# Kernel tuning notes

Hardware: AMD Instinct MI355X
Metric: run time of the kernel (lower is better)

## Reference

```python
import jax, jax.numpy as jnp
import numpy as np

B, T, C = 2, 2048, 2048
H, G, HS = 16, 4, 128       # n_head, n_query_groups, head_size
N_ELEM = 128                # rotary_percentage * head_size
D_FF = 4 * C
EPS = 1e-5


def layer_norm(x, w, b):
    mu = jnp.mean(x, axis=-1, keepdims=True)
    var = jnp.var(x, axis=-1, keepdims=True)
    return (x - mu) * jax.lax.rsqrt(var + EPS) * w + b


def apply_rope(x, cos, sin):
    # x: (B, H, T, n_elem); cos/sin: (T, n_elem) with freqs duplicated over halves
    half = x.shape[-1] // 2
    x1, x2 = x[..., :half], x[..., half:]
    rotated = jnp.concatenate((-x2, x1), axis=-1)
    return x * cos + rotated * sin


def setup_inputs() -> dict:
    key = jax.random.key(0)
    ks = jax.random.split(key, 8)
    x = jax.random.normal(ks[0], (B, T, C), dtype=jnp.float32)
    # RoPE cache (neox/llama style, duplicated halves to match half-rotation apply_rope)
    inv_freq = 1.0 / (10000.0 ** (jnp.arange(0, N_ELEM, 2, dtype=jnp.float32) / N_ELEM))
    freqs = jnp.outer(jnp.arange(T, dtype=jnp.float32), inv_freq)  # (T, n_elem/2)
    cos = jnp.concatenate((jnp.cos(freqs), jnp.cos(freqs)), axis=-1)
    sin = jnp.concatenate((jnp.sin(freqs), jnp.sin(freqs)), axis=-1)
    mask = jnp.tril(jnp.ones((T, T), dtype=bool))
    s = 0.02
    qkv_w = jax.random.normal(ks[1], ((H + 2 * G) * HS, C), dtype=jnp.float32) * s
    proj_w = jax.random.normal(ks[2], (C, C), dtype=jnp.float32) * s
    fc1_w = jax.random.normal(ks[3], (D_FF, C), dtype=jnp.float32) * s
    fc2_w = jax.random.normal(ks[4], (C, D_FF), dtype=jnp.float32) * s
    return {
        "x": x, "cos": cos, "sin": sin, "mask": mask,
        "ln1_w": jnp.ones((C,), jnp.float32), "ln1_b": jnp.zeros((C,), jnp.float32),
        "qkv_w": qkv_w, "proj_w": proj_w,
        "ln2_w": jnp.ones((C,), jnp.float32), "ln2_b": jnp.zeros((C,), jnp.float32),
        "fc1_w": fc1_w, "fc1_b": jnp.zeros((D_FF,), jnp.float32),
        "fc2_w": fc2_w, "fc2_b": jnp.zeros((C,), jnp.float32),
    }


def block_forward(x, cos, sin, mask, ln1_w, ln1_b, qkv_w, proj_w,
                  ln2_w, ln2_b, fc1_w, fc1_b, fc2_w, fc2_b):
    q_per_kv = H // G
    # --- LayerNormLinear: LN then fused QKV projection ---
    qkv = layer_norm(x, ln1_w, ln1_b) @ qkv_w.T            # (B, T, (H+2G)*HS)
    qkv = qkv.reshape(B, T, G, q_per_kv + 2, HS).transpose(0, 2, 3, 1, 4)
    q = qkv[:, :, :q_per_kv]                               # (B, G, q_per_kv, T, HS)
    k = qkv[:, :, q_per_kv:q_per_kv + 1]                   # (B, G, 1, T, HS)
    v = qkv[:, :, q_per_kv + 1:]
    # GQA expansion (repeat_interleave over the per-group axis)
    k = jnp.repeat(k, q_per_kv, axis=2)
    v = jnp.repeat(v, q_per_kv, axis=2)
    q = q.reshape(B, H, T, HS)
    k = k.reshape(B, H, T, HS)
    v = v.reshape(B, H, T, HS)
    # --- RoPE on first N_ELEM channels ---
    q = jnp.concatenate((apply_rope(q[..., :N_ELEM], cos, sin), q[..., N_ELEM:]), axis=-1)
    k = jnp.concatenate((apply_rope(k[..., :N_ELEM], cos, sin), k[..., N_ELEM:]), axis=-1)
    # --- SDPA with boolean mask ---
    scale = 1.0 / jnp.sqrt(jnp.asarray(HS, q.dtype))
    att = jnp.einsum("bhqd,bhkd->bhqk", q, k) * scale
    att = jnp.where(mask, att, jnp.finfo(att.dtype).min)
    att = jax.nn.softmax(att, axis=-1)
    y = jnp.einsum("bhqk,bhkd->bhqd", att, v)
    y = y.transpose(0, 2, 1, 3).reshape(B, T, C)
    h = y @ proj_w.T
    # --- non-parallel residual: x += attn; x += MLP(LN(x)) ---
    x = x + h
    mlp = jax.nn.gelu(layer_norm(x, ln2_w, ln2_b) @ fc1_w.T + fc1_b, approximate=False)
    x = x + (mlp @ fc2_w.T + fc2_b)
    return x


def reference(x, cos, sin, mask, ln1_w, ln1_b, qkv_w, proj_w,
              ln2_w, ln2_b, fc1_w, fc1_b, fc2_w, fc2_b):
    return block_forward(x, cos, sin, mask, ln1_w, ln1_b, qkv_w, proj_w,
                         ln2_w, ln2_b, fc1_w, fc1_b, fc2_w, fc2_b)
```

## Files before the change

### kernel.cpp

```cpp
#include <hip/hip_runtime.h>

typedef __bf16 bf16;
typedef __bf16 bf16x8 __attribute__((ext_vector_type(8)));
typedef __bf16 bf16x4 __attribute__((ext_vector_type(4)));
typedef float  f32x4  __attribute__((ext_vector_type(4)));

#define LOG2E 1.4426950408889634f

__device__ __forceinline__ void gload_lds16(const void* g, void* l) {
    __builtin_amdgcn_global_load_lds(
        (__attribute__((address_space(1))) const void*)g,
        (__attribute__((address_space(3))) void*)l, 16, 0, 0);
}

__global__ __launch_bounds__(256) void cvt_bf16(const float* __restrict__ src,
                                                bf16* __restrict__ dst, int n) {
    int i = (blockIdx.x * 256 + threadIdx.x) * 4;
    if (i + 3 < n) {
        float4 v = *(const float4*)(src + i);
        bf16x4 o;
        o[0] = (bf16)v.x; o[1] = (bf16)v.y; o[2] = (bf16)v.z; o[3] = (bf16)v.w;
        *(bf16x4*)(dst + i) = o;
    }
}

__global__ __launch_bounds__(256) void ln_kernel(const float* __restrict__ x,
                                                 const float* __restrict__ wgt,
                                                 const float* __restrict__ bias,
                                                 bf16* __restrict__ out) {
    __shared__ float red[8];
    const int tid = threadIdx.x;
    const int lane = tid & 63, w = tid >> 6;
    const size_t row = blockIdx.x;
    const float4* xr = (const float4*)(x + row * 2048);
    float4 v0 = xr[tid];
    float4 v1 = xr[tid + 256];
    float s = v0.x + v0.y + v0.z + v0.w + v1.x + v1.y + v1.z + v1.w;
    float q = v0.x*v0.x + v0.y*v0.y + v0.z*v0.z + v0.w*v0.w
            + v1.x*v1.x + v1.y*v1.y + v1.z*v1.z + v1.w*v1.w;
    #pragma unroll
    for (int off = 32; off; off >>= 1) {
        s += __shfl_xor(s, off);
        q += __shfl_xor(q, off);
    }
    if (lane == 0) { red[w] = s; red[4 + w] = q; }
    __syncthreads();
    float S  = red[0] + red[1] + red[2] + red[3];
    float Q2 = red[4] + red[5] + red[6] + red[7];
    float mu = S * (1.0f / 2048.0f);
    float var = Q2 * (1.0f / 2048.0f) - mu * mu;
    float rstd = rsqrtf(var + 1e-5f);

    bf16* orow = out + row * 2048;
    int c0 = tid * 4;
    float vv[8] = {v0.x, v0.y, v0.z, v0.w, v1.x, v1.y, v1.z, v1.w};
    bf16x4 o;
    #pragma unroll
    for (int k = 0; k < 4; ++k)
        o[k] = (bf16)((vv[k] - mu) * rstd * wgt[c0 + k] + bias[c0 + k]);
    *(bf16x4*)(orow + c0) = o;
    #pragma unroll
    for (int k = 0; k < 4; ++k)
        o[k] = (bf16)((vv[4 + k] - mu) * rstd * wgt[1024 + c0 + k] + bias[1024 + c0 + k]);
    *(bf16x4*)(orow + 1024 + c0) = o;
}

template <int EPI>
__global__ __launch_bounds__(512, 4) void gemmB(const bf16* __restrict__ A,
                                                const bf16* __restrict__ B,
                                                void* __restrict__ OutP,
                                                const float* __restrict__ bias,
                                                const float* __restrict__ res,
                                                int M, int N, int K) {
    __shared__ __align__(16) char lds[65536];
    const int tid = threadIdx.x;
    const int lane = tid & 63;
    const int w = tid >> 6, wr = w >> 1, wc = w & 1;
    const int lo = lane & 15, hi = lane >> 4;

    const int nwg = gridDim.x;
    const int bid = blockIdx.x;
    const int q = nwg >> 3, r = nwg & 7, xcd = bid & 7, off = bid >> 3;
    const int s = (xcd < r ? xcd * (q + 1) : r * (q + 1) + (xcd - r) * q) + off;
    const int MB = M / 128;
    const int per = MB * 4;
    const int grp = s / per, t2 = s - grp * per;
    const int brow = (t2 % MB) * 128;
    const int bcol = (grp * 4 + t2 / MB) * 128;

    const int sr = tid >> 3;
    const int su = (tid & 7) ^ (sr & 7);
    const bf16* Ag = A + (size_t)(brow + sr) * K + su * 8;
    const bf16* Bg = B + (size_t)(bcol + sr) * K + su * 8;
    const size_t K64 = (size_t)64 * K;
    char* dst0 = lds + tid * 16;

    auto stage = [&](int bf, int kt) {
        char* d = dst0 + bf * 32768;
        gload_lds16(Ag + kt * 64, d);
        gload_lds16(Ag + K64 + kt * 64, d + 8192);
        gload_lds16(Bg + kt * 64, d + 16384);
        gload_lds16(Bg + K64 + kt * 64, d + 24576);
    };

    f32x4 acc[2][4] = {};
    const int NT = K >> 6;

    stage(0, 0);
    for (int kt = 0; kt < NT; ++kt) {
        const int cur = kt & 1;
        if (kt + 1 < NT) {
            stage(cur ^ 1, kt + 1);
            asm volatile("s_waitcnt vmcnt(4)" ::: "memory");
        } else {
            asm volatile("s_waitcnt vmcnt(0)" ::: "memory");
        }
        __builtin_amdgcn_s_barrier();

        const char* ab = lds + cur * 32768;
        const char* bb = ab + 16384;
        bf16x8 af[2][2], bfv[4][2];
        #pragma unroll
        for (int m = 0; m < 2; ++m) {
            const int rA = wr * 32 + m * 16 + lo;
            #pragma unroll
            for (int ks = 0; ks < 2; ++ks)
                af[m][ks] = *(const bf16x8*)(ab + rA * 128 + (((ks * 4 + hi) ^ (lo & 7)) << 4));
        }
        #pragma unroll
        for (int n = 0; n < 4; ++n) {
            const int rB = wc * 64 + n * 16 + lo;
            #pragma unroll
            for (int ks = 0; ks < 2; ++ks)
                bfv[n][ks] = *(const bf16x8*)(bb + rB * 128 + (((ks * 4 + hi) ^ (lo & 7)) << 4));
        }
        __builtin_amdgcn_s_setprio(1);
        #pragma unroll
        for (int m = 0; m < 2; ++m)
            #pragma unroll
            for (int n = 0; n < 4; ++n)
                #pragma unroll
                for (int ks = 0; ks < 2; ++ks)
                    acc[m][n] = __builtin_amdgcn_mfma_f32_16x16x32_bf16(af[m][ks], bfv[n][ks], acc[m][n], 0, 0, 0);
        __builtin_amdgcn_s_setprio(0);
        __builtin_amdgcn_s_barrier();
    }

    float* outF = (float*)OutP;
    bf16*  outB = (bf16*)OutP;
    #pragma unroll
    for (int n = 0; n < 4; ++n) {
        const int col = bcol + wc * 64 + n * 16 + lo;
        float bv = 0.f;
        if (EPI == 1 || EPI == 3) bv = bias[col];
        #pragma unroll
        for (int m = 0; m < 2; ++m) {
            #pragma unroll
            for (int rr = 0; rr < 4; ++rr) {
                const int row = brow + wr * 32 + m * 16 + hi * 4 + rr;
                float v = acc[m][n][rr];
                if (EPI == 0) {
                    outB[(size_t)row * N + col] = (bf16)v;
                } else if (EPI == 1) {
                    v += bv;
                    v = 0.5f * v * (1.0f + erff(v * 0.70710678118654752f));
                    outB[(size_t)row * N + col] = (bf16)v;
                } else if (EPI == 2) {
                    outF[(size_t)row * N + col] = res[(size_t)row * N + col] + v;
                } else {
                    outF[(size_t)row * N + col] = res[(size_t)row * N + col] + v + bv;
                }
            }
        }
    }
}

__global__ __launch_bounds__(256) void rope_scatter(const bf16* __restrict__ qkv,
                                                    const float* __restrict__ cosb,
                                                    const float* __restrict__ sinb,
                                                    bf16* __restrict__ Q,
                                                    bf16* __restrict__ Kg,
                                                    bf16* __restrict__ Vt) {
    const int tid = threadIdx.x;
    const int row = blockIdx.x;
    const int b = row >> 11, t = row & 2047;
    const bf16* src = qkv + (size_t)row * 3072;
    for (int i = tid; i < 1536; i += 256) {
        int slot = i >> 6;
        int d = i & 63;
        int g = slot / 6, m = slot - g * 6;
        float v1 = (float)src[slot * 128 + d];
        float v2 = (float)src[slot * 128 + d + 64];
        float o1, o2;
        if (m < 5) {
            float c1 = cosb[t * 128 + d],      s1 = sinb[t * 128 + d];
            float c2 = cosb[t * 128 + d + 64], s2 = sinb[t * 128 + d + 64];
            o1 = v1 * c1 - v2 * s1;
            o2 = v2 * c2 + v1 * s2;
        } else {
            o1 = v1; o2 = v2;
        }
        if (m < 4) {
            int hh = g * 4 + m;
            size_t base = ((size_t)(b * 16 + hh) * 2048 + t) * 128;
            Q[base + d] = (bf16)o1;
            Q[base + d + 64] = (bf16)o2;
        } else if (m == 4) {
            size_t base = ((size_t)(b * 4 + g) * 2048 + t) * 128;
            Kg[base + d] = (bf16)o1;
            Kg[base + d + 64] = (bf16)o2;
        } else {
            size_t base = (size_t)(b * 4 + g) * 128;
            Vt[(base + d) * 2048 + t] = (bf16)o1;
            Vt[(base + d + 64) * 2048 + t] = (bf16)o2;
        }
    }
}

__global__ __launch_bounds__(256) void attn_kernel(const bf16* __restrict__ Q,
                                                   const bf16* __restrict__ Kg,
                                                   const bf16* __restrict__ Vt,
                                                   bf16* __restrict__ Y) {
    __shared__ __align__(16) bf16 Ks[64 * 128];
    __shared__ __align__(16) bf16 Vs[128 * 64];
    __shared__ __align__(16) bf16 Ps[4][16 * 80];

    const int tid = threadIdx.x;
    const int lane = tid & 63, w = tid >> 6;
    const int lo = lane & 15, hi = lane >> 4;
    const int bh = blockIdx.y;
    const int b = bh >> 4, h = bh & 15;
    const int g = h >> 2;

    const bf16* Kbase = Kg + (size_t)(b * 4 + g) * 2048 * 128;
    const bf16* Vbase = Vt + (size_t)(b * 4 + g) * 128 * 2048;
    const float scale = 0.08838834764831845f;
    bf16* pw = &Ps[w][0];

    #pragma unroll 1
    for (int pass = 0; pass < 2; ++pass) {
        const int qt = pass ? 31 - (int)blockIdx.x : (int)blockIdx.x;
        const int q0 = qt * 64;

        bf16x8 qf[4];
        {
            const size_t qbase = ((size_t)bh * 2048 + q0 + w * 16 + lo) * 128;
            #pragma unroll
            for (int dd = 0; dd < 4; ++dd)
                qf[dd] = *(const bf16x8*)(Q + qbase + dd * 32 + hi * 8);
        }

        float m_r[4], l_r[4];
        f32x4 oacc[8] = {};
        #pragma unroll
        for (int rr = 0; rr < 4; ++rr) { m_r[rr] = -1e30f; l_r[rr] = 0.f; }

        for (int kt = 0; kt <= qt; ++kt) {
            #pragma unroll
            for (int it = 0; it < 4; ++it) {
                int ob = (it * 256 + tid) * 16;
                int rk = ob >> 8, cb = ob & 255;
                bf16x8 kv = *(const bf16x8*)(Kbase + (size_t)(kt * 64 + rk) * 128 + (cb >> 1));
                *(bf16x8*)((char*)Ks + rk * 256 + (cb ^ ((rk & 7) << 4))) = kv;
                int dv = ob >> 7, cv = ob & 127;
                bf16x8 vv = *(const bf16x8*)(Vbase + (size_t)dv * 2048 + kt * 64 + (cv >> 1));
                *(bf16x8*)((char*)Vs + dv * 128 + (cv ^ ((dv & 7) << 4))) = vv;
            }
            __syncthreads();

            f32x4 sj[4];
            #pragma unroll
            for (int j = 0; j < 4; ++j) {
                f32x4 a = {};
                int rk = j * 16 + lo;
                #pragma unroll
                for (int dd = 0; dd < 4; ++dd) {
                    int cb = dd * 64 + hi * 16;
                    bf16x8 kf = *(const bf16x8*)((const char*)Ks + rk * 256 + (cb ^ ((rk & 7) << 4)));
                    a = __builtin_amdgcn_mfma_f32_16x16x32_bf16(qf[dd], kf, a, 0, 0, 0);
                }
                sj[j] = a;
            }

            float sv[4][4];
            const bool diag = (kt == qt);
            #pragma unroll
            for (int j = 0; j < 4; ++j)
                #pragma unroll
                for (int rr = 0; rr < 4; ++rr) {
                    float v = sj[j][rr] * scale;
                    if (diag) {
                        int tg = kt * 64 + j * 16 + lo;
                        int qg = q0 + w * 16 + hi * 4 + rr;
                        if (tg > qg) v = -1e30f;
                    }
                    sv[j][rr] = v;
                }

            float mx[4];
            #pragma unroll
            for (int rr = 0; rr < 4; ++rr) {
                float m0 = fmaxf(fmaxf(sv[0][rr], sv[1][rr]), fmaxf(sv[2][rr], sv[3][rr]));
                #pragma unroll
                for (int off = 8; off; off >>= 1) m0 = fmaxf(m0, __shfl_xor(m0, off, 16));
                mx[rr] = m0;
            }
            float p[4][4];
            float rs[4], al[4];
            #pragma unroll
            for (int rr = 0; rr < 4; ++rr) {
                float mnew = fmaxf(m_r[rr], mx[rr]);
                #pragma unroll
                for (int j = 0; j < 4; ++j)
                    p[j][rr] = exp2f((sv[j][rr] - mnew) * LOG2E);
                float s0 = p[0][rr] + p[1][rr] + p[2][rr] + p[3][rr];
                #pragma unroll
                for (int off = 8; off; off >>= 1) s0 += __shfl_xor(s0, off, 16);
                rs[rr] = s0;
                al[rr] = exp2f((m_r[rr] - mnew) * LOG2E);
                l_r[rr] = l_r[rr] * al[rr] + rs[rr];
                m_r[rr] = mnew;
            }
            #pragma unroll
            for (int dn = 0; dn < 8; ++dn)
                #pragma unroll
                for (int rr = 0; rr < 4; ++rr) oacc[dn][rr] *= al[rr];

            #pragma unroll
            for (int j = 0; j < 4; ++j)
                #pragma unroll
                for (int rr = 0; rr < 4; ++rr)
                    pw[(hi * 4 + rr) * 80 + j * 16 + lo] = (bf16)p[j][rr];

            #pragma unroll
            for (int tc = 0; tc < 2; ++tc) {
                bf16x8 pf = *(const bf16x8*)(pw + lo * 80 + tc * 32 + hi * 8);
                #pragma unroll
                for (int dn = 0; dn < 8; ++dn) {
                    int rv = dn * 16 + lo;
                    int cv = tc * 64 + hi * 16;
                    bf16x8 vf = *(const bf16x8*)((const char*)Vs + rv * 128 + (cv ^ ((rv & 7) << 4)));
                    oacc[dn] = __builtin_amdgcn_mfma_f32_16x16x32_bf16(pf, vf, oacc[dn], 0, 0, 0);
                }
            }
            __syncthreads();
        }

        #pragma unroll
        for (int dn = 0; dn < 8; ++dn)
            #pragma unroll
            for (int rr = 0; rr < 4; ++rr) {
                int qg = q0 + w * 16 + hi * 4 + rr;
                Y[((size_t)b * 2048 + qg) * 2048 + h * 128 + dn * 16 + lo] =
                    (bf16)(oacc[dn][rr] / l_r[rr]);
            }
    }
}

extern "C" void kernel_launch(void* const* d_in, const int* in_sizes, int n_in,
                              void* d_out, int out_size, void* d_ws, size_t ws_size,
                              hipStream_t stream) {
    const float* x      = (const float*)d_in[0];
    const float* cosb   = (const float*)d_in[1];
    const float* sinb   = (const float*)d_in[2];
    const float* ln1_w  = (const float*)d_in[4];
    const float* ln1_b  = (const float*)d_in[5];
    const float* qkv_w  = (const float*)d_in[6];
    const float* proj_w = (const float*)d_in[7];
    const float* ln2_w  = (const float*)d_in[8];
    const float* ln2_b  = (const float*)d_in[9];
    const float* fc1_w  = (const float*)d_in[10];
    const float* fc1_b  = (const float*)d_in[11];
    const float* fc2_w  = (const float*)d_in[12];
    const float* fc2_b  = (const float*)d_in[13];
    float* out = (float*)d_out;

    char* ws = (char*)d_ws;
    bf16*  w_qkv  = (bf16*)(ws + 0ull);
    bf16*  w_proj = (bf16*)(ws + 12582912ull);
    bf16*  w_fc1  = (bf16*)(ws + 20971520ull);
    bf16*  w_fc2  = (bf16*)(ws + 54525952ull);
    float* x2     = (float*)(ws + 88080384ull);
    bf16*  lnout  = (bf16*)(ws + 121634816ull);
    char*  R      = ws + 138412032ull;
    bf16*  qkvo = (bf16*)(R);
    bf16*  Qb   = (bf16*)(R + 25165824ull);
    bf16*  Kb   = (bf16*)(R + 41943040ull);
    bf16*  Vtb  = (bf16*)(R + 46137344ull);
    bf16*  Yb   = (bf16*)(R + 50331648ull);
    bf16*  mlp  = (bf16*)(R);

    cvt_bf16<<<6144,  256, 0, stream>>>(qkv_w,  w_qkv,  3072 * 2048);
    cvt_bf16<<<4096,  256, 0, stream>>>(proj_w, w_proj, 2048 * 2048);
    cvt_bf16<<<16384, 256, 0, stream>>>(fc1_w,  w_fc1,  8192 * 2048);
    cvt_bf16<<<16384, 256, 0, stream>>>(fc2_w,  w_fc2,  2048 * 8192);

    ln_kernel<<<4096, 256, 0, stream>>>(x, ln1_w, ln1_b, lnout);

    gemmB<0><<<768, 512, 0, stream>>>(lnout, w_qkv, qkvo, nullptr, nullptr,
                                      4096, 3072, 2048);

    rope_scatter<<<4096, 256, 0, stream>>>(qkvo, cosb, sinb, Qb, Kb, Vtb);

    attn_kernel<<<dim3(16, 32), 256, 0, stream>>>(Qb, Kb, Vtb, Yb);

    gemmB<2><<<512, 512, 0, stream>>>(Yb, w_proj, x2, nullptr, x,
                                      4096, 2048, 2048);

    ln_kernel<<<4096, 256, 0, stream>>>(x2, ln2_w, ln2_b, lnout);

    gemmB<1><<<2048, 512, 0, stream>>>(lnout, w_fc1, mlp, fc1_b, nullptr,
                                       4096, 8192, 2048);

    gemmB<3><<<512, 512, 0, stream>>>(mlp, w_fc2, out, fc2_b, x2,
                                      4096, 2048, 8192);
}
```

Baseline: 716.7 us.

## Add 256x256 ping-pong GEMM with split-K for fc2 and use it for QKV/fc1/fc2

Introduces a new GEMM kernel with 256x256 tiles, 128KB dynamic LDS double buffering, explicit barrier/waitcnt interleaving of LDS reads, global-to-LDS loads and MFMA quarters, plus s_setprio around MFMA bursts. It replaces the previous GEMM for the QKV, fc1 and fc2 projections. fc2 is split into two K halves across blockIdx.y, with the second half written to a scratch buffer and summed by a separate add kernel. The goal is more data reuse per tile and better latency hiding, and the split-K keeps fc2's small grid filling the GPU. The cost is an extra fp32 pass for the split-K reduction, reduced occupancy, and reuse of the fc1 weight workspace as scratch.

```diff
diff --git a/kernel.cpp b/kernel.cpp
--- a/kernel.cpp
+++ b/kernel.cpp
@@ -12,6 +12,16 @@
         (__attribute__((address_space(1))) const void*)g,
         (__attribute__((address_space(3))) void*)l, 16, 0, 0);
 }
+
+template <int N> __device__ __forceinline__ void vmwait() {
+    if constexpr (N == 0) asm volatile("s_waitcnt vmcnt(0)" ::: "memory");
+    else if constexpr (N == 4) asm volatile("s_waitcnt vmcnt(4)" ::: "memory");
+}
+
+#define BARA() { asm volatile("" ::: "memory"); __builtin_amdgcn_s_barrier(); \
+    asm volatile("s_waitcnt lgkmcnt(0)" ::: "memory"); __builtin_amdgcn_sched_barrier(0); }
+#define BARB() { asm volatile("" ::: "memory"); __builtin_amdgcn_s_barrier(); \
+    asm volatile("" ::: "memory"); }
 
 __global__ __launch_bounds__(256) void cvt_bf16(const float* __restrict__ src,
                                                 bf16* __restrict__ dst, int n) {
@@ -21,6 +31,17 @@
         bf16x4 o;
         o[0] = (bf16)v.x; o[1] = (bf16)v.y; o[2] = (bf16)v.z; o[3] = (bf16)v.w;
         *(bf16x4*)(dst + i) = o;
+    }
+}
+
+__global__ __launch_bounds__(256) void add_f32(float* __restrict__ out,
+                                               const float* __restrict__ p, int n) {
+    int i = (blockIdx.x * 256 + threadIdx.x) * 4;
+    if (i + 3 < n) {
+        float4 a = *(const float4*)(out + i);
+        float4 b = *(const float4*)(p + i);
+        a.x += b.x; a.y += b.y; a.z += b.z; a.w += b.w;
+        *(float4*)(out + i) = a;
     }
 }
 
@@ -63,6 +84,141 @@
     for (int k = 0; k < 4; ++k)
         o[k] = (bf16)((vv[4 + k] - mu) * rstd * wgt[1024 + c0 + k] + bias[1024 + c0 + k]);
     *(bf16x4*)(orow + 1024 + c0) = o;
+}
+
+template <int EPI>
+__global__ __launch_bounds__(512, 2) void gemmP(const bf16* __restrict__ A,
+                                                const bf16* __restrict__ B,
+                                                void* __restrict__ OutP,
+                                                const float* __restrict__ bias,
+                                                const float* __restrict__ res,
+                                                float* __restrict__ Aux,
+                                                int M, int N, int Kc,
+                                                int lda, int ldb) {
+    extern __shared__ __align__(16) char lds[];
+    const int tid = threadIdx.x;
+    const int lane = tid & 63;
+    const int w = tid >> 6, wr = w >> 2, wc = w & 3;
+    const int lo = lane & 15, hi = lane >> 4;
+    const int ln16 = lane * 16;
+    const int koff = (EPI == 5) ? (int)blockIdx.y * Kc : 0;
+
+    const int nwg = gridDim.x;
+    const int bid = blockIdx.x;
+    const int q = nwg >> 3, r = nwg & 7, xcd = bid & 7, off = bid >> 3;
+    const int s = (xcd < r ? xcd * (q + 1) : r * (q + 1) + (xcd - r) * q) + off;
+    const int MB = M / 256;
+    const int per = MB * 4;
+    const int grp = s / per, t2 = s - grp * per;
+    const int brow = (t2 % MB) * 256;
+    const int bcol = (grp * 4 + t2 / MB) * 256;
+
+    const bf16* Asrc = A + (size_t)(brow + w * 16 + lo) * lda + koff + hi * 8;
+    const bf16* Bsrc = B + (size_t)(bcol + w * 16 + lo) * ldb + koff + hi * 8;
+
+    auto stA = [&](int bf, int kt, int h) {
+        const bf16* g = Asrc + (size_t)h * 128 * lda + kt * 64;
+        char* d = lds + bf * 65536 + h * 16384 + (w << 10) + ln16;
+        gload_lds16(g, d);
+        gload_lds16(g + 32, d + 8192);
+    };
+    auto stB = [&](int bf, int kt, int h) {
+        const bf16* g = Bsrc + (size_t)h * 128 * ldb + kt * 64;
+        char* d = lds + bf * 65536 + 32768 + h * 16384 + (w << 10) + ln16;
+        gload_lds16(g, d);
+        gload_lds16(g + 32, d + 8192);
+    };
+
+    bf16x8 af[4][2], b0[2][2], b1[2][2];
+    f32x4 acc[8][4] = {};
+
+#define LDA(BF, MH) { _Pragma("unroll") for (int mm = 0; mm < 4; ++mm) { \
+    _Pragma("unroll") for (int ks = 0; ks < 2; ++ks) { \
+        af[mm][ks] = *(const bf16x8*)(lds + (BF) * 65536 + wr * 16384 + \
+                                      ((ks * 8 + (MH) * 4 + mm) << 10) + ln16); } } }
+#define LDB(BF, NH, RG) { _Pragma("unroll") for (int nn = 0; nn < 2; ++nn) { \
+    _Pragma("unroll") for (int ks = 0; ks < 2; ++ks) { \
+        RG[nn][ks] = *(const bf16x8*)(lds + (BF) * 65536 + 32768 + (wc >> 1) * 16384 + \
+                                      ((ks * 8 + (wc & 1) * 4 + (NH) * 2 + nn) << 10) + ln16); } } }
+#define MFMAQ(MH, NH, RG) { __builtin_amdgcn_s_setprio(1); \
+    _Pragma("unroll") for (int mm = 0; mm < 4; ++mm) { \
+    _Pragma("unroll") for (int nn = 0; nn < 2; ++nn) { \
+    _Pragma("unroll") for (int ks = 0; ks < 2; ++ks) { \
+        acc[(MH) * 4 + mm][(NH) * 2 + nn] = __builtin_amdgcn_mfma_f32_16x16x32_bf16( \
+            af[mm][ks], RG[nn][ks], acc[(MH) * 4 + mm][(NH) * 2 + nn], 0, 0, 0); } } } \
+    __builtin_amdgcn_s_setprio(0); }
+
+    const int NT = Kc >> 6;
+    const int NIT = NT >> 1;
+
+    stA(0, 0, 0); stA(0, 0, 1);
+    stB(0, 0, 0); stB(0, 0, 1);
+    stA(1, 1, 0); stA(1, 1, 1);
+    vmwait<4>();
+    BARB();
+
+    #pragma unroll 1
+    for (int T = 0; T < NIT - 1; ++T) {
+        const int t = 2 * T;
+        LDA(0, 0) LDB(0, 0, b0) stB(1, t + 1, 0); stB(1, t + 1, 1);
+        BARA(); MFMAQ(0, 0, b0) BARB();
+        LDB(0, 1, b1)  BARA(); MFMAQ(0, 1, b1) BARB();
+        LDA(0, 1)      BARA(); MFMAQ(1, 1, b1) BARB();
+        LDB(0, 0, b0)  stA(0, t + 2, 0); stA(0, t + 2, 1); vmwait<4>();
+        BARA(); MFMAQ(1, 0, b0) BARB();
+        LDA(1, 0) LDB(1, 0, b0) stB(0, t + 2, 0); stB(0, t + 2, 1);
+        BARA(); MFMAQ(0, 0, b0) BARB();
+        LDB(1, 1, b1)  BARA(); MFMAQ(0, 1, b1) BARB();
+        LDA(1, 1)      BARA(); MFMAQ(1, 1, b1) BARB();
+        LDB(1, 0, b0)  stA(1, t + 3, 0); stA(1, t + 3, 1); vmwait<4>();
+        BARA(); MFMAQ(1, 0, b0) BARB();
+    }
+    {
+        LDA(0, 0) LDB(0, 0, b0) stB(1, NT - 1, 0); stB(1, NT - 1, 1);
+        BARA(); MFMAQ(0, 0, b0) BARB();
+        LDB(0, 1, b1)  BARA(); MFMAQ(0, 1, b1) BARB();
+        LDA(0, 1)      BARA(); MFMAQ(1, 1, b1) BARB();
+        LDB(0, 0, b0)  vmwait<0>();
+        BARA(); MFMAQ(1, 0, b0) BARB();
+        LDA(1, 0) LDB(1, 0, b0) BARA(); MFMAQ(0, 0, b0) BARB();
+        LDB(1, 1, b1)  BARA(); MFMAQ(0, 1, b1) BARB();
+        LDA(1, 1)      BARA(); MFMAQ(1, 1, b1) BARB();
+        LDB(1, 0, b0)  BARA(); MFMAQ(1, 0, b0)
+    }
+#undef LDA
+#undef LDB
+#undef MFMAQ
+
+    float* outF = (float*)OutP;
+    bf16*  outB = (bf16*)OutP;
+    #pragma unroll
+    for (int n = 0; n < 4; ++n) {
+        const int col = bcol + wc * 64 + n * 16 + lo;
+        float bv = 0.f;
+        if (EPI == 1 || EPI == 3 || EPI == 5) bv = bias[col];
+        #pragma unroll
+        for (int m = 0; m < 8; ++m) {
+            #pragma unroll
+            for (int rr = 0; rr < 4; ++rr) {
+                const int row = brow + wr * 128 + m * 16 + hi * 4 + rr;
+                float v = acc[m][n][rr];
+                if (EPI == 0) {
+                    outB[(size_t)row * N + col] = (bf16)v;
+                } else if (EPI == 1) {
+                    v += bv;
+                    v = 0.5f * v * (1.0f + erff(v * 0.70710678118654752f));
+                    outB[(size_t)row * N + col] = (bf16)v;
+                } else if (EPI == 3) {
+                    outF[(size_t)row * N + col] = res[(size_t)row * N + col] + v + bv;
+                } else if (EPI == 5) {
+                    if (blockIdx.y == 0)
+                        outF[(size_t)row * N + col] = res[(size_t)row * N + col] + v + bv;
+                    else
+                        Aux[(size_t)row * N + col] = v;
+                }
+            }
+        }
+    }
 }
 
 template <int EPI>
@@ -389,6 +545,7 @@
     bf16*  Vtb  = (bf16*)(R + 46137344ull);
     bf16*  Yb   = (bf16*)(R + 50331648ull);
     bf16*  mlp  = (bf16*)(R);
+    float* p1   = (float*)(ws + 20971520ull);
 
     cvt_bf16<<<6144,  256, 0, stream>>>(qkv_w,  w_qkv,  3072 * 2048);
     cvt_bf16<<<4096,  256, 0, stream>>>(proj_w, w_proj, 2048 * 2048);
@@ -397,8 +554,8 @@
 
     ln_kernel<<<4096, 256, 0, stream>>>(x, ln1_w, ln1_b, lnout);
 
-    gemmB<0><<<768, 512, 0, stream>>>(lnout, w_qkv, qkvo, nullptr, nullptr,
-                                      4096, 3072, 2048);
+    gemmP<0><<<dim3(192, 1), 512, 131072, stream>>>(lnout, w_qkv, qkvo, nullptr, nullptr,
+                                                    nullptr, 4096, 3072, 2048, 2048, 2048);
 
     rope_scatter<<<4096, 256, 0, stream>>>(qkvo, cosb, sinb, Qb, Kb, Vtb);
 
@@ -409,9 +566,10 @@
 
     ln_kernel<<<4096, 256, 0, stream>>>(x2, ln2_w, ln2_b, lnout);
 
-    gemmB<1><<<2048, 512, 0, stream>>>(lnout, w_fc1, mlp, fc1_b, nullptr,
-                                       4096, 8192, 2048);
-
-    gemmB<3><<<512, 512, 0, stream>>>(mlp, w_fc2, out, fc2_b, x2,
-                                      4096, 2048, 8192);
-}
+    gemmP<1><<<dim3(512, 1), 512, 131072, stream>>>(lnout, w_fc1, mlp, fc1_b, nullptr,
+                                                    nullptr, 4096, 8192, 2048, 2048, 2048);
+
+    gemmP<5><<<dim3(128, 2), 512, 131072, stream>>>(mlp, w_fc2, out, fc2_b, x2,
+                                                    p1, 4096, 2048, 4096, 8192, 8192);
+    add_f32<<<8192, 256, 0, stream>>>(out, p1, 4096 * 2048);
+}
```

New measurement: 754.9 us. +5.3%, slower.

## Use 256x256-tile GEMM for FC1 and split V transpose into dedicated kernel

Applied to the files above, without the earlier changes.

Adds a new GEMM kernel with 256x256 output tiles, 8x4 MFMA accumulators per wave, double-buffered direct-to-LDS loads, XCD-aware block remapping and setprio around MFMA bursts. It replaces the FC1+GELU GEMM, aiming for more operand reuse and fewer workgroups. Separately, the V transpose moves out of rope_scatter into a kernel that writes 16-byte vector stores instead of strided scalar scatters. The large tile raises register pressure and uses 64KB of LDS per block, which may limit occupancy.

```diff
diff --git a/kernel.cpp b/kernel.cpp
--- a/kernel.cpp
+++ b/kernel.cpp
@@ -175,45 +175,157 @@
     }
 }
 
+template <int EPI>
+__global__ __launch_bounds__(512, 2) void gemmE(const bf16* __restrict__ A,
+                                                const bf16* __restrict__ B,
+                                                void* __restrict__ OutP,
+                                                const float* __restrict__ bias,
+                                                int M, int N, int K) {
+    extern __shared__ __align__(16) char lds[];
+    const int tid = threadIdx.x;
+    const int lane = tid & 63;
+    const int w = tid >> 6, wr = w >> 2, wc = w & 3;
+    const int lo = lane & 15, hi = lane >> 4;
+
+    const int nwg = gridDim.x;
+    const int bid = blockIdx.x;
+    const int q = nwg >> 3, r = nwg & 7, xcd = bid & 7, off = bid >> 3;
+    const int s = (xcd < r ? xcd * (q + 1) : r * (q + 1) + (xcd - r) * q) + off;
+    const int MB = M / 256;
+    const int per = MB * 4;
+    const int grp = s / per, t2 = s - grp * per;
+    const int brow = (t2 % MB) * 256;
+    const int bcol = (grp * 4 + t2 / MB) * 256;
+
+    const int srow = tid >> 2;
+    const int scol = ((tid & 3) ^ ((tid >> 3) & 3)) * 8;
+    const bf16* Ag = A + (size_t)(brow + srow) * K + scol;
+    const bf16* Bg = B + (size_t)(bcol + srow) * K + scol;
+    const size_t R128 = (size_t)128 * K;
+    char* d0 = lds + tid * 16;
+
+    auto stage = [&](int bf, int kt) {
+        char* d = d0 + bf * 32768;
+        gload_lds16(Ag + kt * 32, d);
+        gload_lds16(Ag + R128 + kt * 32, d + 8192);
+        gload_lds16(Bg + kt * 32, d + 16384);
+        gload_lds16(Bg + R128 + kt * 32, d + 24576);
+    };
+
+    f32x4 acc[8][4] = {};
+    const int NT = K >> 5;
+    const int xsl = (hi ^ ((lo >> 1) & 3)) << 4;
+
+    stage(0, 0);
+    #pragma unroll 1
+    for (int kt = 0; kt < NT; ++kt) {
+        const int cur = kt & 1;
+        if (kt + 1 < NT) {
+            stage(cur ^ 1, kt + 1);
+            asm volatile("s_waitcnt vmcnt(4)" ::: "memory");
+        } else {
+            asm volatile("s_waitcnt vmcnt(0)" ::: "memory");
+        }
+        __builtin_amdgcn_s_barrier();
+
+        const char* ab = lds + cur * 32768;
+        const char* bb = ab + 16384;
+        bf16x8 af[8], bv[4];
+        #pragma unroll
+        for (int m = 0; m < 4; ++m)
+            af[m] = *(const bf16x8*)(ab + (wr * 128 + m * 16 + lo) * 64 + xsl);
+        #pragma unroll
+        for (int n = 0; n < 4; ++n)
+            bv[n] = *(const bf16x8*)(bb + (wc * 64 + n * 16 + lo) * 64 + xsl);
+        __builtin_amdgcn_s_setprio(1);
+        #pragma unroll
+        for (int m = 0; m < 4; ++m)
+            #pragma unroll
+            for (int n = 0; n < 4; ++n)
+                acc[m][n] = __builtin_amdgcn_mfma_f32_16x16x32_bf16(af[m], bv[n], acc[m][n], 0, 0, 0);
+        __builtin_amdgcn_s_setprio(0);
+        #pragma unroll
+        for (int m = 4; m < 8; ++m)
+            af[m] = *(const bf16x8*)(ab + (wr * 128 + m * 16 + lo) * 64 + xsl);
+        __builtin_amdgcn_s_setprio(1);
+        #pragma unroll
+        for (int m = 4; m < 8; ++m)
+            #pragma unroll
+            for (int n = 0; n < 4; ++n)
+                acc[m][n] = __builtin_amdgcn_mfma_f32_16x16x32_bf16(af[m], bv[n], acc[m][n], 0, 0, 0);
+        __builtin_amdgcn_s_setprio(0);
+        __builtin_amdgcn_s_barrier();
+    }
+
+    bf16* outB = (bf16*)OutP;
+    #pragma unroll
+    for (int n = 0; n < 4; ++n) {
+        const int col = bcol + wc * 64 + n * 16 + lo;
+        float bv2 = bias[col];
+        #pragma unroll
+        for (int m = 0; m < 8; ++m) {
+            #pragma unroll
+            for (int rr = 0; rr < 4; ++rr) {
+                const int row = brow + wr * 128 + m * 16 + hi * 4 + rr;
+                float v = acc[m][n][rr] + bv2;
+                v = 0.5f * v * (1.0f + erff(v * 0.70710678118654752f));
+                outB[(size_t)row * N + col] = (bf16)v;
+            }
+        }
+    }
+}
+
 __global__ __launch_bounds__(256) void rope_scatter(const bf16* __restrict__ qkv,
                                                     const float* __restrict__ cosb,
                                                     const float* __restrict__ sinb,
                                                     bf16* __restrict__ Q,
-                                                    bf16* __restrict__ Kg,
-                                                    bf16* __restrict__ Vt) {
+                                                    bf16* __restrict__ Kg) {
     const int tid = threadIdx.x;
     const int row = blockIdx.x;
     const int b = row >> 11, t = row & 2047;
     const bf16* src = qkv + (size_t)row * 3072;
-    for (int i = tid; i < 1536; i += 256) {
+    #pragma unroll
+    for (int i = tid; i < 1280; i += 256) {
         int slot = i >> 6;
         int d = i & 63;
-        int g = slot / 6, m = slot - g * 6;
-        float v1 = (float)src[slot * 128 + d];
-        float v2 = (float)src[slot * 128 + d + 64];
-        float o1, o2;
-        if (m < 5) {
-            float c1 = cosb[t * 128 + d],      s1 = sinb[t * 128 + d];
-            float c2 = cosb[t * 128 + d + 64], s2 = sinb[t * 128 + d + 64];
-            o1 = v1 * c1 - v2 * s1;
-            o2 = v2 * c2 + v1 * s2;
-        } else {
-            o1 = v1; o2 = v2;
-        }
+        int g = slot / 5, m = slot - g * 5;
+        int msrc = g * 6 + m;
+        float v1 = (float)src[msrc * 128 + d];
+        float v2 = (float)src[msrc * 128 + d + 64];
+        float c1 = cosb[t * 128 + d],      s1 = sinb[t * 128 + d];
+        float c2 = cosb[t * 128 + d + 64], s2 = sinb[t * 128 + d + 64];
+        float o1 = v1 * c1 - v2 * s1;
+        float o2 = v2 * c2 + v1 * s2;
         if (m < 4) {
             int hh = g * 4 + m;
             size_t base = ((size_t)(b * 16 + hh) * 2048 + t) * 128;
             Q[base + d] = (bf16)o1;
             Q[base + d + 64] = (bf16)o2;
-        } else if (m == 4) {
+        } else {
             size_t base = ((size_t)(b * 4 + g) * 2048 + t) * 128;
             Kg[base + d] = (bf16)o1;
             Kg[base + d + 64] = (bf16)o2;
-        } else {
-            size_t base = (size_t)(b * 4 + g) * 128;
-            Vt[(base + d) * 2048 + t] = (bf16)o1;
-            Vt[(base + d + 64) * 2048 + t] = (bf16)o2;
-        }
+        }
+    }
+}
+
+__global__ __launch_bounds__(256) void vtrans(const bf16* __restrict__ qkvo,
+                                              bf16* __restrict__ Vt) {
+    const int tid = threadIdx.x;
+    const int t0 = blockIdx.x * 64;
+    const int z  = blockIdx.y;
+    const int b = z >> 2, g = z & 3;
+    const int d = tid & 127;
+    const int th = tid >> 7;
+    const bf16* src = qkvo + (size_t)(b * 2048 + t0 + th * 32) * 3072 + g * 768 + 640 + d;
+    bf16* dst = Vt + ((size_t)z * 128 + d) * 2048 + t0 + th * 32;
+    #pragma unroll
+    for (int c = 0; c < 4; ++c) {
+        bf16x8 v;
+        #pragma unroll
+        for (int j = 0; j < 8; ++j)
+            v[j] = src[(size_t)(c * 8 + j) * 3072];
+        *(bf16x8*)(dst + c * 8) = v;
     }
 }
 
@@ -390,6 +502,8 @@
     bf16*  Yb   = (bf16*)(R + 50331648ull);
     bf16*  mlp  = (bf16*)(R);
 
+    constexpr int LDSE = 65536;
+
     cvt_bf16<<<6144,  256, 0, stream>>>(qkv_w,  w_qkv,  3072 * 2048);
     cvt_bf16<<<4096,  256, 0, stream>>>(proj_w, w_proj, 2048 * 2048);
     cvt_bf16<<<16384, 256, 0, stream>>>(fc1_w,  w_fc1,  8192 * 2048);
@@ -400,7 +514,8 @@
     gemmB<0><<<768, 512, 0, stream>>>(lnout, w_qkv, qkvo, nullptr, nullptr,
                                       4096, 3072, 2048);
 
-    rope_scatter<<<4096, 256, 0, stream>>>(qkvo, cosb, sinb, Qb, Kb, Vtb);
+    rope_scatter<<<4096, 256, 0, stream>>>(qkvo, cosb, sinb, Qb, Kb);
+    vtrans<<<dim3(32, 8), 256, 0, stream>>>(qkvo, Vtb);
 
     attn_kernel<<<dim3(16, 32), 256, 0, stream>>>(Qb, Kb, Vtb, Yb);
 
@@ -409,8 +524,8 @@
 
     ln_kernel<<<4096, 256, 0, stream>>>(x2, ln2_w, ln2_b, lnout);
 
-    gemmB<1><<<2048, 512, 0, stream>>>(lnout, w_fc1, mlp, fc1_b, nullptr,
-                                       4096, 8192, 2048);
+    gemmE<1><<<512, 512, LDSE, stream>>>(lnout, w_fc1, mlp, fc1_b,
+                                         4096, 8192, 2048);
 
     gemmB<3><<<512, 512, 0, stream>>>(mlp, w_fc2, out, fc2_b, x2,
                                       4096, 2048, 8192);
```

After: 706.6 us. Within noise of the previous version (-1.4%).

## Double-buffer attention K/V tiles, lazy softmax rescale, split V transpose kernel

Applied to the files above, without the earlier changes.

The attention kernel now double-buffers K and V in LDS. It prefetches the next tile into registers while computing the current one, which drops one barrier per iteration and hides global load latency. The online softmax now rescales the accumulator only when a row max grows by more than a threshold. This skips exp and multiply work on most tiles, at the cost of slightly different numerics that should still stay bounded. The strided V-transpose writes are moved out of rope_scatter into a separate vtrans kernel that writes contiguous 16-byte chunks, at the cost of one extra kernel launch.

```diff
diff --git a/kernel.cpp b/kernel.cpp
--- a/kernel.cpp
+++ b/kernel.cpp
@@ -179,41 +179,53 @@
                                                     const float* __restrict__ cosb,
                                                     const float* __restrict__ sinb,
                                                     bf16* __restrict__ Q,
-                                                    bf16* __restrict__ Kg,
-                                                    bf16* __restrict__ Vt) {
+                                                    bf16* __restrict__ Kg) {
     const int tid = threadIdx.x;
     const int row = blockIdx.x;
     const int b = row >> 11, t = row & 2047;
     const bf16* src = qkv + (size_t)row * 3072;
-    for (int i = tid; i < 1536; i += 256) {
+    #pragma unroll
+    for (int i = tid; i < 1280; i += 256) {
         int slot = i >> 6;
         int d = i & 63;
-        int g = slot / 6, m = slot - g * 6;
-        float v1 = (float)src[slot * 128 + d];
-        float v2 = (float)src[slot * 128 + d + 64];
-        float o1, o2;
-        if (m < 5) {
-            float c1 = cosb[t * 128 + d],      s1 = sinb[t * 128 + d];
-            float c2 = cosb[t * 128 + d + 64], s2 = sinb[t * 128 + d + 64];
-            o1 = v1 * c1 - v2 * s1;
-            o2 = v2 * c2 + v1 * s2;
-        } else {
-            o1 = v1; o2 = v2;
-        }
+        int g = slot / 5, m = slot - g * 5;
+        int msrc = g * 6 + m;
+        float v1 = (float)src[msrc * 128 + d];
+        float v2 = (float)src[msrc * 128 + d + 64];
+        float c1 = cosb[t * 128 + d],      s1 = sinb[t * 128 + d];
+        float c2 = cosb[t * 128 + d + 64], s2 = sinb[t * 128 + d + 64];
+        float o1 = v1 * c1 - v2 * s1;
+        float o2 = v2 * c2 + v1 * s2;
         if (m < 4) {
             int hh = g * 4 + m;
             size_t base = ((size_t)(b * 16 + hh) * 2048 + t) * 128;
             Q[base + d] = (bf16)o1;
             Q[base + d + 64] = (bf16)o2;
-        } else if (m == 4) {
+        } else {
             size_t base = ((size_t)(b * 4 + g) * 2048 + t) * 128;
             Kg[base + d] = (bf16)o1;
             Kg[base + d + 64] = (bf16)o2;
-        } else {
-            size_t base = (size_t)(b * 4 + g) * 128;
-            Vt[(base + d) * 2048 + t] = (bf16)o1;
-            Vt[(base + d + 64) * 2048 + t] = (bf16)o2;
-        }
+        }
+    }
+}
+
+__global__ __launch_bounds__(256) void vtrans(const bf16* __restrict__ qkvo,
+                                              bf16* __restrict__ Vt) {
+    const int tid = threadIdx.x;
+    const int t0 = blockIdx.x * 64;
+    const int z  = blockIdx.y;
+    const int b = z >> 2, g = z & 3;
+    const int d = tid & 127;
+    const int th = tid >> 7;
+    const bf16* src = qkvo + (size_t)(b * 2048 + t0 + th * 32) * 3072 + g * 768 + 640 + d;
+    bf16* dst = Vt + ((size_t)z * 128 + d) * 2048 + t0 + th * 32;
+    #pragma unroll
+    for (int c = 0; c < 4; ++c) {
+        bf16x8 v;
+        #pragma unroll
+        for (int j = 0; j < 8; ++j)
+            v[j] = src[(size_t)(c * 8 + j) * 3072];
+        *(bf16x8*)(dst + c * 8) = v;
     }
 }
 
@@ -221,8 +233,8 @@
                                                    const bf16* __restrict__ Kg,
                                                    const bf16* __restrict__ Vt,
                                                    bf16* __restrict__ Y) {
-    __shared__ __align__(16) bf16 Ks[64 * 128];
-    __shared__ __align__(16) bf16 Vs[128 * 64];
+    __shared__ __align__(16) bf16 Ks[2][64 * 128];
+    __shared__ __align__(16) bf16 Vs[2][128 * 64];
     __shared__ __align__(16) bf16 Ps[4][16 * 80];
 
     const int tid = threadIdx.x;
@@ -237,6 +249,8 @@
     const float scale = 0.08838834764831845f;
     bf16* pw = &Ps[w][0];
 
+    bf16x8 kreg[4], vreg[4];
+
     #pragma unroll 1
     for (int pass = 0; pass < 2; ++pass) {
         const int qt = pass ? 31 - (int)blockIdx.x : (int)blockIdx.x;
@@ -255,18 +269,40 @@
         #pragma unroll
         for (int rr = 0; rr < 4; ++rr) { m_r[rr] = -1e30f; l_r[rr] = 0.f; }
 
+        #pragma unroll
+        for (int it = 0; it < 4; ++it) {
+            int ob = (it * 256 + tid) * 16;
+            int rk = ob >> 8, cb = ob & 255;
+            kreg[it] = *(const bf16x8*)(Kbase + (size_t)rk * 128 + (cb >> 1));
+            int dv = ob >> 7, cv = ob & 127;
+            vreg[it] = *(const bf16x8*)(Vbase + (size_t)dv * 2048 + (cv >> 1));
+        }
+        #pragma unroll
+        for (int it = 0; it < 4; ++it) {
+            int ob = (it * 256 + tid) * 16;
+            int rk = ob >> 8, cb = ob & 255;
+            *(bf16x8*)((char*)Ks[0] + rk * 256 + (cb ^ ((rk & 7) << 4))) = kreg[it];
+            int dv = ob >> 7, cv = ob & 127;
+            *(bf16x8*)((char*)Vs[0] + dv * 128 + (cv ^ ((dv & 7) << 4))) = vreg[it];
+        }
+        __syncthreads();
+        int cur = 0;
+
         for (int kt = 0; kt <= qt; ++kt) {
-            #pragma unroll
-            for (int it = 0; it < 4; ++it) {
-                int ob = (it * 256 + tid) * 16;
-                int rk = ob >> 8, cb = ob & 255;
-                bf16x8 kv = *(const bf16x8*)(Kbase + (size_t)(kt * 64 + rk) * 128 + (cb >> 1));
-                *(bf16x8*)((char*)Ks + rk * 256 + (cb ^ ((rk & 7) << 4))) = kv;
-                int dv = ob >> 7, cv = ob & 127;
-                bf16x8 vv = *(const bf16x8*)(Vbase + (size_t)dv * 2048 + kt * 64 + (cv >> 1));
-                *(bf16x8*)((char*)Vs + dv * 128 + (cv ^ ((dv & 7) << 4))) = vv;
-            }
-            __syncthreads();
+            const bool pf = (kt < qt);
+            if (pf) {
+                #pragma unroll
+                for (int it = 0; it < 4; ++it) {
+                    int ob = (it * 256 + tid) * 16;
+                    int rk = ob >> 8, cb = ob & 255;
+                    kreg[it] = *(const bf16x8*)(Kbase + (size_t)((kt + 1) * 64 + rk) * 128 + (cb >> 1));
+                    int dv = ob >> 7, cv = ob & 127;
+                    vreg[it] = *(const bf16x8*)(Vbase + (size_t)dv * 2048 + (kt + 1) * 64 + (cv >> 1));
+                }
+            }
+
+            const char* KsC = (const char*)Ks[cur];
+            const char* VsC = (const char*)Vs[cur];
 
             f32x4 sj[4];
             #pragma unroll
@@ -276,7 +312,7 @@
                 #pragma unroll
                 for (int dd = 0; dd < 4; ++dd) {
                     int cb = dd * 64 + hi * 16;
-                    bf16x8 kf = *(const bf16x8*)((const char*)Ks + rk * 256 + (cb ^ ((rk & 7) << 4)));
+                    bf16x8 kf = *(const bf16x8*)(KsC + rk * 256 + (cb ^ ((rk & 7) << 4)));
                     a = __builtin_amdgcn_mfma_f32_16x16x32_bf16(qf[dd], kf, a, 0, 0, 0);
                 }
                 sj[j] = a;
@@ -305,26 +341,33 @@
                 for (int off = 8; off; off >>= 1) m0 = fmaxf(m0, __shfl_xor(m0, off, 16));
                 mx[rr] = m0;
             }
+
+            bool need = false;
+            #pragma unroll
+            for (int rr = 0; rr < 4; ++rr) need = need || (mx[rr] > m_r[rr] + 8.0f);
+            if (__any(need)) {
+                #pragma unroll
+                for (int rr = 0; rr < 4; ++rr) {
+                    float mnew = fmaxf(m_r[rr], mx[rr]);
+                    float al = exp2f((m_r[rr] - mnew) * LOG2E);
+                    l_r[rr] *= al;
+                    m_r[rr] = mnew;
+                    #pragma unroll
+                    for (int dn = 0; dn < 8; ++dn) oacc[dn][rr] *= al;
+                }
+            }
+
             float p[4][4];
-            float rs[4], al[4];
             #pragma unroll
             for (int rr = 0; rr < 4; ++rr) {
-                float mnew = fmaxf(m_r[rr], mx[rr]);
                 #pragma unroll
                 for (int j = 0; j < 4; ++j)
-                    p[j][rr] = exp2f((sv[j][rr] - mnew) * LOG2E);
+                    p[j][rr] = exp2f((sv[j][rr] - m_r[rr]) * LOG2E);
                 float s0 = p[0][rr] + p[1][rr] + p[2][rr] + p[3][rr];
                 #pragma unroll
                 for (int off = 8; off; off >>= 1) s0 += __shfl_xor(s0, off, 16);
-                rs[rr] = s0;
-                al[rr] = exp2f((m_r[rr] - mnew) * LOG2E);
-                l_r[rr] = l_r[rr] * al[rr] + rs[rr];
-                m_r[rr] = mnew;
-            }
-            #pragma unroll
-            for (int dn = 0; dn < 8; ++dn)
-                #pragma unroll
-                for (int rr = 0; rr < 4; ++rr) oacc[dn][rr] *= al[rr];
+                l_r[rr] += s0;
+            }
 
             #pragma unroll
             for (int j = 0; j < 4; ++j)
@@ -334,16 +377,28 @@
 
             #pragma unroll
             for (int tc = 0; tc < 2; ++tc) {
-                bf16x8 pf = *(const bf16x8*)(pw + lo * 80 + tc * 32 + hi * 8);
+                bf16x8 pf2 = *(const bf16x8*)(pw + lo * 80 + tc * 32 + hi * 8);
                 #pragma unroll
                 for (int dn = 0; dn < 8; ++dn) {
                     int rv = dn * 16 + lo;
                     int cv = tc * 64 + hi * 16;
-                    bf16x8 vf = *(const bf16x8*)((const char*)Vs + rv * 128 + (cv ^ ((rv & 7) << 4)));
-                    oacc[dn] = __builtin_amdgcn_mfma_f32_16x16x32_bf16(pf, vf, oacc[dn], 0, 0, 0);
+                    bf16x8 vf = *(const bf16x8*)(VsC + rv * 128 + (cv ^ ((rv & 7) << 4)));
+                    oacc[dn] = __builtin_amdgcn_mfma_f32_16x16x32_bf16(pf2, vf, oacc[dn], 0, 0, 0);
+                }
+            }
+
+            if (pf) {
+                #pragma unroll
+                for (int it = 0; it < 4; ++it) {
+                    int ob = (it * 256 + tid) * 16;
+                    int rk = ob >> 8, cb = ob & 255;
+                    *(bf16x8*)((char*)Ks[cur ^ 1] + rk * 256 + (cb ^ ((rk & 7) << 4))) = kreg[it];
+                    int dv = ob >> 7, cv = ob & 127;
+                    *(bf16x8*)((char*)Vs[cur ^ 1] + dv * 128 + (cv ^ ((dv & 7) << 4))) = vreg[it];
                 }
             }
             __syncthreads();
+            cur ^= 1;
         }
 
         #pragma unroll
@@ -400,7 +455,8 @@
     gemmB<0><<<768, 512, 0, stream>>>(lnout, w_qkv, qkvo, nullptr, nullptr,
                                       4096, 3072, 2048);
 
-    rope_scatter<<<4096, 256, 0, stream>>>(qkvo, cosb, sinb, Qb, Kb, Vtb);
+    rope_scatter<<<4096, 256, 0, stream>>>(qkvo, cosb, sinb, Qb, Kb);
+    vtrans<<<dim3(32, 8), 256, 0, stream>>>(qkvo, Vtb);
 
     attn_kernel<<<dim3(16, 32), 256, 0, stream>>>(Qb, Kb, Vtb, Yb);
 
```

Measured after the change: 671.1 us. 1.07x faster.
